# Kernel optimization log

Measured on AMD Instinct MI355X. Metric: run time of the kernel, lower is better.

The kernel has to match this reference:

```python
import jax, jax.numpy as jnp
import numpy as np

NEG_SLOPE = 0.2
RECON_W = 0.1
BN_EPS = 1e-5


def gat_conv(x, edge_index, W, a_src, a_dst, b):
    """PyG-style GATConv (eval mode, add_self_loops=True, concat heads).
    x: [N, F_in], W: [F_in, H*C], a_src/a_dst: [H, C], b: [H*C]."""
    N = x.shape[0]
    H, C = a_src.shape
    h = (x @ W).reshape(N, H, C)                      # [N,H,C]
    loop = jnp.arange(N, dtype=edge_index.dtype)
    src = jnp.concatenate([edge_index[0], loop])
    dst = jnp.concatenate([edge_index[1], loop])
    alpha_src = jnp.sum(h * a_src, axis=-1)           # [N,H]
    alpha_dst = jnp.sum(h * a_dst, axis=-1)           # [N,H]
    e = jax.nn.leaky_relu(alpha_src[src] + alpha_dst[dst], NEG_SLOPE)  # [E,H]
    # segment softmax over incoming edges of each destination node
    m = jax.ops.segment_max(e, dst, num_segments=N)
    e = jnp.exp(e - m[dst])
    s = jax.ops.segment_sum(e, dst, num_segments=N)
    p = e / s[dst]                                    # [E,H]
    out = jax.ops.segment_sum(p[:, :, None] * h[src], dst, num_segments=N)  # [N,H,C]
    return out.reshape(N, H * C) + b


def setup_inputs() -> dict:
    key = jax.random.key(0)
    ks = jax.random.split(key, 24)
    N, E = 100000, 800000
    F_in, hid, heads, n_cls, ctx_d, expl_d = 128, 32, 4, 10, 6, 32
    HC = hid * heads  # 128
    g = lambda k, shp, sc=0.1: jax.random.normal(k, shp, dtype=jnp.float32) * sc
    return {
        "x": jax.random.normal(ks[0], (N, F_in), dtype=jnp.float32),
        "edge_index": jax.random.randint(ks[1], (2, E), 0, N, dtype=jnp.int32),
        "context": jax.random.normal(ks[2], (N, ctx_d), dtype=jnp.float32),
        # GATConv 1: F_in -> hid, heads
        "W1": g(ks[3], (F_in, HC)), "a_src1": g(ks[4], (heads, hid)),
        "a_dst1": g(ks[5], (heads, hid)), "b1": g(ks[6], (HC,)),
        # BatchNorm1d(HC), eval mode
        "bn_gamma": jnp.ones((HC,), jnp.float32), "bn_beta": g(ks[7], (HC,)),
        "bn_mean": g(ks[8], (HC,)), "bn_var": jax.random.uniform(ks[9], (HC,), jnp.float32, 0.5, 1.5),
        # GATConv 2: HC -> hid, 1 head
        "W2": g(ks[10], (HC, hid)), "a_src2": g(ks[11], (1, hid)),
        "a_dst2": g(ks[12], (1, hid)), "b2": g(ks[13], (hid,)),
        # Reasoner MLP: ctx_d -> hid -> expl_d
        "rw1": g(ks[14], (ctx_d, hid)), "rb1": g(ks[15], (hid,)),
        "rw2": g(ks[16], (hid, expl_d)), "rb2": g(ks[17], (expl_d,)),
        # Decoder: expl_d -> hid
        "dw": g(ks[18], (expl_d, hid)), "db": g(ks[19], (hid,)),
        # Classifier: hid -> n_cls
        "cw": g(ks[20], (hid, n_cls)), "cb": g(ks[21], (n_cls,)),
    }


def reference(x, edge_index, context, W1, a_src1, a_dst1, b1,
              bn_gamma, bn_beta, bn_mean, bn_var,
              W2, a_src2, a_dst2, b2, rw1, rb1, rw2, rb2, dw, db, cw, cb):
    # layer 1: GAT -> BN(eval) -> ELU (dropout inactive in eval)
    h = gat_conv(x, edge_index, W1, a_src1, a_dst1, b1)
    h = (h - bn_mean) * jax.lax.rsqrt(bn_var + BN_EPS) * bn_gamma + bn_beta
    h = jax.nn.elu(h)
    # layer 2: GAT (1 head)
    h = gat_conv(h, edge_index, W2, a_src2, a_dst2, b2)  # [N, hid]
    # reasoner + decoder
    expl = jnp.maximum(context @ rw1 + rb1, 0.0) @ rw2 + rb2   # [N, expl_d]
    recon = expl @ dw + db                                     # [N, hid]
    combined = h + RECON_W * recon
    logits = combined @ cw + cb
    return jax.nn.log_softmax(logits, axis=1), expl
```

## Files before the change

### kernel.cpp

```cpp
#include <hip/hip_runtime.h>
#include <hip/hip_bf16.h>
#include <math.h>

#define NEG_SLOPE 0.2f
#define RECON_W 0.1f
#define BN_EPS 1e-5f
#define CAP 64

typedef __attribute__((ext_vector_type(8))) short short8;
typedef __attribute__((ext_vector_type(4))) float f32x4;

__device__ __forceinline__ float lrelu(float v) {
    return (v >= 0.f) ? v : NEG_SLOPE * v;
}
__device__ __forceinline__ unsigned short f2bf(float f) {
    unsigned int u = __float_as_uint(f);
    u = (u + 0x7fffu + ((u >> 16) & 1u)) >> 16;
    return (unsigned short)u;
}
__device__ __forceinline__ float bf2f(unsigned short u) {
    return __uint_as_float(((unsigned int)u) << 16);
}
__device__ __forceinline__ unsigned int pack2bf(float a, float b) {
    return (unsigned int)f2bf(a) | ((unsigned int)f2bf(b) << 16);
}
__device__ __forceinline__ void unpack2(unsigned int u, float& a, float& b) {
    a = bf2f((unsigned short)u);
    b = bf2f((unsigned short)(u >> 16));
}

__global__ __launch_bounds__(256) void prep_kernel(
    const float* __restrict__ W1, const float* __restrict__ W2,
    const float* __restrict__ b1, const float* __restrict__ g,
    const float* __restrict__ be, const float* __restrict__ m, const float* __restrict__ v,
    unsigned short* __restrict__ w1t, unsigned short* __restrict__ w2t,
    float* __restrict__ bnsc, float* __restrict__ bnsh) {
    int b = blockIdx.x, tid = threadIdx.x;
    if (b < 64) {
        int e = b * 256 + tid;
        w1t[e] = f2bf(W1[(e & 127) * 128 + (e >> 7)]);
    } else {
        #pragma unroll
        for (int it = 0; it < 16; it++) {
            int e = it * 256 + tid;
            w2t[e] = f2bf(W2[(e & 127) * 32 + (e >> 7)]);
        }
        if (tid < 128) {
            float s = rsqrtf(v[tid] + BN_EPS) * g[tid];
            bnsc[tid] = s;
            bnsh[tid] = (b1[tid] - m[tid]) * s + be[tid];
        }
    }
}

__global__ __launch_bounds__(256) void gemm1_mfma_kernel(
    const float* __restrict__ x, const unsigned short* __restrict__ w1t,
    const float* __restrict__ a_src, const float* __restrict__ a_dst,
    unsigned short* __restrict__ h1g, float* __restrict__ as1, float* __restrict__ ad1, int N,
    const int* __restrict__ esrc, const int* __restrict__ edst, int E,
    int* __restrict__ cnt, int* __restrict__ csrS) {
    __shared__ unsigned short sA[64 * 128];
    __shared__ unsigned short sBt[128 * 128];
    __shared__ float s_as[128], s_ad[128];
    int tid = threadIdx.x;
    int rowBase = blockIdx.x * 64;

    int bs0 = -1, bs1 = -1, bd0 = 0, bd1 = 0, bp0 = CAP, bp1 = CAP;
    int nb = gridDim.x;
    int epb = (E + nb - 1) / nb;
    int e0 = blockIdx.x * epb;
    int e1 = min(e0 + epb, E);
    {
        int e = e0 + tid;
        if (e < e1) { bs0 = esrc[e]; bd0 = edst[e]; }
        if (e + 256 < e1) { bs1 = esrc[e + 256]; bd1 = edst[e + 256]; }
        if (bs0 >= 0) bp0 = atomicAdd(&cnt[bd0], 1);
        if (bs1 >= 0) bp1 = atomicAdd(&cnt[bd1], 1);
    }

    if (tid < 128) { s_as[tid] = a_src[tid]; s_ad[tid] = a_dst[tid]; }
    #pragma unroll
    for (int u = 0; u < 8; u++) {
        int f = tid + u * 256;
        int r = f >> 5, cg = f & 31;
        int gr = rowBase + r;
        float4 vv = make_float4(0.f, 0.f, 0.f, 0.f);
        if (gr < N) vv = *(const float4*)(x + (size_t)gr * 128 + cg * 4);
        uint2 pk;
        pk.x = pack2bf(vv.x, vv.y);
        pk.y = pack2bf(vv.z, vv.w);
        ((uint2*)sA)[f] = pk;
    }
    #pragma unroll
    for (int u = 0; u < 8; u++) {
        int f = tid + u * 256;
        ((uint4*)sBt)[f] = ((const uint4*)w1t)[f];
    }
    __syncthreads();

    int lane = tid & 63;
    int w = tid >> 6;
    int quad = lane >> 4;
    int m16 = lane & 15;

    f32x4 acc[8];
    #pragma unroll
    for (int t = 0; t < 8; t++) acc[t] = (f32x4){0.f, 0.f, 0.f, 0.f};

    #pragma unroll
    for (int kc = 0; kc < 4; kc++) {
        int k0 = kc * 32 + quad * 8;
        short8 af = *(const short8*)(sA + ((w * 16 + m16) * 128 + k0));
        #pragma unroll
        for (int t = 0; t < 8; t++) {
            short8 bf = *(const short8*)(sBt + ((t * 16 + m16) * 128 + k0));
            acc[t] = __builtin_amdgcn_mfma_f32_16x16x32_bf16(af, bf, acc[t], 0, 0, 0);
        }
    }

    #pragma unroll
    for (int t = 0; t < 8; t++) {
        #pragma unroll
        for (int r = 0; r < 4; r++) {
            int row = w * 16 + quad * 4 + r;
            int col = t * 16 + m16;
            sA[row * 128 + col] = f2bf(acc[t][r]);
        }
    }
    __syncthreads();
    #pragma unroll
    for (int u = 0; u < 8; u++) {
        int f = tid + u * 256;
        int r = f >> 5, cg = f & 31;
        int gr = rowBase + r;
        if (gr < N) *(uint2*)(h1g + (size_t)gr * 128 + cg * 4) = ((const uint2*)sA)[f];
    }
    {
        int row = tid >> 2, head = tid & 3;
        int gr = rowBase + row;
        if (gr < N) {
            const unsigned int* rowp = (const unsigned int*)(sA + row * 128);
            float ps = 0.f, pd = 0.f;
            #pragma unroll
            for (int j = 0; j < 16; j++) {
                float f0, f1;
                unpack2(rowp[head * 16 + j], f0, f1);
                int c = head * 32 + j * 2;
                ps = fmaf(f0, s_as[c], fmaf(f1, s_as[c + 1], ps));
                pd = fmaf(f0, s_ad[c], fmaf(f1, s_ad[c + 1], pd));
            }
            as1[gr * 4 + head] = ps;
            ad1[gr * 4 + head] = pd;
        }
    }
    if (bs0 >= 0 && bp0 < CAP) csrS[(size_t)bd0 * CAP + bp0] = bs0;
    if (bs1 >= 0 && bp1 < CAP) csrS[(size_t)bd1 * CAP + bp1] = bs1;
    for (int e = e0 + tid + 512; e < e1; e += 256) {
        int s = esrc[e], d = edst[e];
        int pos = atomicAdd(&cnt[d], 1);
        if (pos < CAP) csrS[(size_t)d * CAP + pos] = s;
    }
}

__global__ __launch_bounds__(256) void agg1_kernel(
    const unsigned short* __restrict__ h1g,
    const float* __restrict__ as1, const float* __restrict__ ad1,
    const int* __restrict__ cnt, const int* __restrict__ csrS,
    const float* __restrict__ bnscale, const float* __restrict__ bnshift,
    unsigned short* __restrict__ h1p, int N) {
    __shared__ int   sSrc[16][CAP + 1];
    __shared__ float sW[16][CAP + 1][4];
    int tid = threadIdx.x;
    int nid = tid >> 4;
    int l   = tid & 15;
    int n = blockIdx.x * 16 + nid;
    bool alive = (n < N);
    int total = 0;

    if (alive) {
        int deg = min(cnt[n], CAP);
        total = deg + 1;
        float4 ad4 = *(const float4*)(ad1 + (size_t)n * 4);
        for (int slot = l; slot < total; slot += 16) {
            int s = (slot < deg) ? csrS[n * CAP + slot] : n;
            sSrc[nid][slot] = s;
            float4 a = *(const float4*)(as1 + (size_t)s * 4);
            float4 w4;
            w4.x = __expf(lrelu(a.x + ad4.x));
            w4.y = __expf(lrelu(a.y + ad4.y));
            w4.z = __expf(lrelu(a.z + ad4.z));
            w4.w = __expf(lrelu(a.w + ad4.w));
            *(float4*)(&sW[nid][slot][0]) = w4;
        }
    }
    __syncthreads();
    if (!alive) return;

    int hl = l >> 2;
    unsigned choff = (unsigned)(l << 3);
    const int* sS = sSrc[nid];
    const float* sWp = &sW[nid][0][0];

    float pa0 = 0.f, pa1 = 0.f, pa2 = 0.f, pa3 = 0.f;
    float pa4 = 0.f, pa5 = 0.f, pa6 = 0.f, pa7 = 0.f;
    float pb0 = 0.f, pb1 = 0.f, pb2 = 0.f, pb3 = 0.f;
    float pb4 = 0.f, pb5 = 0.f, pb6 = 0.f, pb7 = 0.f;
    float sa = 0.f, sb = 0.f;
    int j = 0;
    for (; j + 1 < total; j += 2) {
        int s0 = sS[j];
        int s1 = sS[j + 1];
        float w0 = sWp[(j << 2) + hl];
        float w1 = sWp[((j + 1) << 2) + hl];
        uint4 u0 = *(const uint4*)(h1g + (((unsigned)s0 << 7) + choff));
        uint4 u1 = *(const uint4*)(h1g + (((unsigned)s1 << 7) + choff));
        float f0, f1;
        unpack2(u0.x, f0, f1); pa0 = fmaf(w0, f0, pa0); pa1 = fmaf(w0, f1, pa1);
        unpack2(u0.y, f0, f1); pa2 = fmaf(w0, f0, pa2); pa3 = fmaf(w0, f1, pa3);
        unpack2(u0.z, f0, f1); pa4 = fmaf(w0, f0, pa4); pa5 = fmaf(w0, f1, pa5);
        unpack2(u0.w, f0, f1); pa6 = fmaf(w0, f0, pa6); pa7 = fmaf(w0, f1, pa7);
        sa += w0;
        unpack2(u1.x, f0, f1); pb0 = fmaf(w1, f0, pb0); pb1 = fmaf(w1, f1, pb1);
        unpack2(u1.y, f0, f1); pb2 = fmaf(w1, f0, pb2); pb3 = fmaf(w1, f1, pb3);
        unpack2(u1.z, f0, f1); pb4 = fmaf(w1, f0, pb4); pb5 = fmaf(w1, f1, pb5);
        unpack2(u1.w, f0, f1); pb6 = fmaf(w1, f0, pb6); pb7 = fmaf(w1, f1, pb7);
        sb += w1;
    }
    if (j < total) {
        int s0 = sS[j];
        float w0 = sWp[(j << 2) + hl];
        uint4 u0 = *(const uint4*)(h1g + (((unsigned)s0 << 7) + choff));
        float f0, f1;
        unpack2(u0.x, f0, f1); pa0 = fmaf(w0, f0, pa0); pa1 = fmaf(w0, f1, pa1);
        unpack2(u0.y, f0, f1); pa2 = fmaf(w0, f0, pa2); pa3 = fmaf(w0, f1, pa3);
        unpack2(u0.z, f0, f1); pa4 = fmaf(w0, f0, pa4); pa5 = fmaf(w0, f1, pa5);
        unpack2(u0.w, f0, f1); pa6 = fmaf(w0, f0, pa6); pa7 = fmaf(w0, f1, pa7);
        sa += w0;
    }
    float inv = 1.f / (sa + sb);
    float4 sc0 = *(const float4*)(bnscale + l * 8);
    float4 sc1 = *(const float4*)(bnscale + l * 8 + 4);
    float4 sh0 = *(const float4*)(bnshift + l * 8);
    float4 sh1 = *(const float4*)(bnshift + l * 8 + 4);
    float o0 = fmaf((pa0 + pb0) * inv, sc0.x, sh0.x);
    float o1 = fmaf((pa1 + pb1) * inv, sc0.y, sh0.y);
    float o2 = fmaf((pa2 + pb2) * inv, sc0.z, sh0.z);
    float o3 = fmaf((pa3 + pb3) * inv, sc0.w, sh0.w);
    float o4 = fmaf((pa4 + pb4) * inv, sc1.x, sh1.x);
    float o5 = fmaf((pa5 + pb5) * inv, sc1.y, sh1.y);
    float o6 = fmaf((pa6 + pb6) * inv, sc1.z, sh1.z);
    float o7 = fmaf((pa7 + pb7) * inv, sc1.w, sh1.w);
    o0 = (o0 > 0.f) ? o0 : expm1f(o0);
    o1 = (o1 > 0.f) ? o1 : expm1f(o1);
    o2 = (o2 > 0.f) ? o2 : expm1f(o2);
    o3 = (o3 > 0.f) ? o3 : expm1f(o3);
    o4 = (o4 > 0.f) ? o4 : expm1f(o4);
    o5 = (o5 > 0.f) ? o5 : expm1f(o5);
    o6 = (o6 > 0.f) ? o6 : expm1f(o6);
    o7 = (o7 > 0.f) ? o7 : expm1f(o7);
    uint4 pk;
    pk.x = pack2bf(o0, o1);
    pk.y = pack2bf(o2, o3);
    pk.z = pack2bf(o4, o5);
    pk.w = pack2bf(o6, o7);
    *(uint4*)(h1p + (size_t)n * 128 + l * 8) = pk;
}

__global__ __launch_bounds__(256) void gemm2_mfma_kernel(
    const unsigned short* __restrict__ A, const unsigned short* __restrict__ w2t,
    const float* __restrict__ a_src, const float* __restrict__ a_dst,
    unsigned short* __restrict__ h2g, float* __restrict__ as2, float* __restrict__ ad2, int N) {
    __shared__ unsigned short sA[64 * 128];
    __shared__ unsigned short sBt[32 * 128];
    __shared__ unsigned short sC[64 * 32];
    __shared__ float s_as[32], s_ad[32];
    int tid = threadIdx.x;
    int rowBase = blockIdx.x * 64;

    if (tid < 32) { s_as[tid] = a_src[tid]; s_ad[tid] = a_dst[tid]; }
    #pragma unroll
    for (int u = 0; u < 4; u++) {
        int f = tid + u * 256;
        int r = f >> 4, g = f & 15;
        int gr = rowBase + r;
        uint4 vv = make_uint4(0, 0, 0, 0);
        if (gr < N) vv = *(const uint4*)(A + (size_t)gr * 128 + g * 8);
        ((uint4*)sA)[f] = vv;
    }
    #pragma unroll
    for (int u = 0; u < 2; u++) {
        int f = tid + u * 256;
        ((uint4*)sBt)[f] = ((const uint4*)w2t)[f];
    }
    __syncthreads();

    int lane = tid & 63;
    int w = tid >> 6;
    int quad = lane >> 4;
    int m16 = lane & 15;

    f32x4 acc[2];
    acc[0] = (f32x4){0.f, 0.f, 0.f, 0.f};
    acc[1] = (f32x4){0.f, 0.f, 0.f, 0.f};
    #pragma unroll
    for (int kc = 0; kc < 4; kc++) {
        int k0 = kc * 32 + quad * 8;
        short8 af = *(const short8*)(sA + ((w * 16 + m16) * 128 + k0));
        #pragma unroll
        for (int t = 0; t < 2; t++) {
            short8 bf = *(const short8*)(sBt + ((t * 16 + m16) * 128 + k0));
            acc[t] = __builtin_amdgcn_mfma_f32_16x16x32_bf16(af, bf, acc[t], 0, 0, 0);
        }
    }
    #pragma unroll
    for (int t = 0; t < 2; t++) {
        #pragma unroll
        for (int r = 0; r < 4; r++) {
            int row = w * 16 + quad * 4 + r;
            sC[row * 32 + t * 16 + m16] = f2bf(acc[t][r]);
        }
    }
    __syncthreads();
    {
        int r = tid >> 2, g = tid & 3;
        int gr = rowBase + r;
        if (gr < N) *(uint4*)(h2g + (size_t)gr * 32 + g * 8) = ((const uint4*)sC)[tid];
    }
    if (tid < 64) {
        int gr = rowBase + tid;
        if (gr < N) {
            const unsigned int* rowp = (const unsigned int*)(sC + tid * 32);
            float ps = 0.f, pd = 0.f;
            #pragma unroll
            for (int j = 0; j < 16; j++) {
                float f0, f1;
                unpack2(rowp[j], f0, f1);
                ps = fmaf(f0, s_as[j * 2], fmaf(f1, s_as[j * 2 + 1], ps));
                pd = fmaf(f0, s_ad[j * 2], fmaf(f1, s_ad[j * 2 + 1], pd));
            }
            as2[gr] = ps;
            ad2[gr] = pd;
        }
    }
}

__global__ __launch_bounds__(256) void agg2_kernel(
    const unsigned short* __restrict__ h2g,
    const float* __restrict__ as2, const float* __restrict__ ad2,
    const int* __restrict__ cnt, const int* __restrict__ csrS,
    const float* __restrict__ b2, float* __restrict__ hl2, int N) {
    __shared__ int   sSrc[32][CAP + 1];
    __shared__ float sW[32][CAP + 1];
    int tid = threadIdx.x;
    int nid = tid >> 3;
    int l   = tid & 7;
    int n = blockIdx.x * 32 + nid;
    bool alive = (n < N);
    int total = 0;

    if (alive) {
        int deg = min(cnt[n], CAP);
        total = deg + 1;
        float ad = ad2[n];
        for (int slot = l; slot < total; slot += 8) {
            int s = (slot < deg) ? csrS[n * CAP + slot] : n;
            sSrc[nid][slot] = s;
            sW[nid][slot] = __expf(lrelu(as2[s] + ad));
        }
    }
    __syncthreads();
    if (!alive) return;

    unsigned choff = (unsigned)(l << 2);
    const int* sS = sSrc[nid];
    const float* sWp = sW[nid];

    float a0a = 0.f, a1a = 0.f, a2a = 0.f, a3a = 0.f, sa = 0.f;
    float a0b = 0.f, a1b = 0.f, a2b = 0.f, a3b = 0.f, sb = 0.f;
    int j = 0;
    for (; j + 1 < total; j += 2) {
        int s0 = sS[j];
        int s1 = sS[j + 1];
        float w0 = sWp[j];
        float w1 = sWp[j + 1];
        uint2 u0 = *(const uint2*)(h2g + (((unsigned)s0 << 5) + choff));
        uint2 u1 = *(const uint2*)(h2g + (((unsigned)s1 << 5) + choff));
        float f0, f1;
        unpack2(u0.x, f0, f1); a0a = fmaf(w0, f0, a0a); a1a = fmaf(w0, f1, a1a);
        unpack2(u0.y, f0, f1); a2a = fmaf(w0, f0, a2a); a3a = fmaf(w0, f1, a3a);
        sa += w0;
        unpack2(u1.x, f0, f1); a0b = fmaf(w1, f0, a0b); a1b = fmaf(w1, f1, a1b);
        unpack2(u1.y, f0, f1); a2b = fmaf(w1, f0, a2b); a3b = fmaf(w1, f1, a3b);
        sb += w1;
    }
    if (j < total) {
        int s0 = sS[j];
        float w0 = sWp[j];
        uint2 u0 = *(const uint2*)(h2g + (((unsigned)s0 << 5) + choff));
        float f0, f1;
        unpack2(u0.x, f0, f1); a0a = fmaf(w0, f0, a0a); a1a = fmaf(w0, f1, a1a);
        unpack2(u0.y, f0, f1); a2a = fmaf(w0, f0, a2a); a3a = fmaf(w0, f1, a3a);
        sa += w0;
    }
    float inv = 1.f / (sa + sb);
    float4 bb = *(const float4*)(b2 + l * 4);
    float4 o;
    o.x = (a0a + a0b) * inv + bb.x;
    o.y = (a1a + a1b) * inv + bb.y;
    o.z = (a2a + a2b) * inv + bb.z;
    o.w = (a3a + a3b) * inv + bb.w;
    *(float4*)(hl2 + (size_t)n * 32 + l * 4) = o;
}

__global__ __launch_bounds__(256) void head_kernel(
    const float* __restrict__ context, const float* __restrict__ hl2,
    const float* __restrict__ rw1, const float* __restrict__ rb1,
    const float* __restrict__ rw2, const float* __restrict__ rb2,
    const float* __restrict__ dw, const float* __restrict__ db,
    const float* __restrict__ cw, const float* __restrict__ cb,
    float* __restrict__ out_lsm, float* __restrict__ out_expl, int N) {
    __shared__ float s_rw1[192], s_rw2[1024], s_dw[1024], s_cw[320];
    __shared__ float s_rb1[32], s_rb2[32], s_db[32], s_cb[10];
    int tid = threadIdx.x;
    for (int i = tid; i < 192; i += 256) s_rw1[i] = rw1[i];
    for (int i = tid; i < 1024; i += 256) { s_rw2[i] = rw2[i]; s_dw[i] = dw[i]; }
    for (int i = tid; i < 320; i += 256) s_cw[i] = cw[i];
    if (tid < 32) { s_rb1[tid] = rb1[tid]; s_rb2[tid] = rb2[tid]; s_db[tid] = db[tid]; }
    if (tid < 10) s_cb[tid] = cb[tid];
    __syncthreads();
    int n = blockIdx.x * 256 + tid;
    if (n >= N) return;

    float ctx[6];
    #pragma unroll
    for (int i = 0; i < 6; i++) ctx[i] = context[(size_t)n * 6 + i];

    float t1[32];
    #pragma unroll
    for (int c = 0; c < 32; c++) t1[c] = s_rb1[c];
    #pragma unroll
    for (int i = 0; i < 6; i++) {
        float s = ctx[i];
        #pragma unroll
        for (int c = 0; c < 32; c++) t1[c] = fmaf(s, s_rw1[i * 32 + c], t1[c]);
    }
    #pragma unroll
    for (int c = 0; c < 32; c++) t1[c] = fmaxf(t1[c], 0.f);

    float ex[32];
    #pragma unroll
    for (int c = 0; c < 32; c++) ex[c] = s_rb2[c];
    #pragma unroll
    for (int c = 0; c < 32; c++) {
        float s = t1[c];
        #pragma unroll
        for (int c2 = 0; c2 < 32; c2++) ex[c2] = fmaf(s, s_rw2[c * 32 + c2], ex[c2]);
    }
    #pragma unroll
    for (int c = 0; c < 32; c += 4)
        *(float4*)(out_expl + (size_t)n * 32 + c) = make_float4(ex[c], ex[c + 1], ex[c + 2], ex[c + 3]);

    float rec[32];
    #pragma unroll
    for (int k = 0; k < 32; k++) rec[k] = s_db[k];
    #pragma unroll
    for (int c = 0; c < 32; c++) {
        float s = ex[c];
        #pragma unroll
        for (int k = 0; k < 32; k++) rec[k] = fmaf(s, s_dw[c * 32 + k], rec[k]);
    }
    float comb[32];
    #pragma unroll
    for (int k = 0; k < 32; k += 4) {
        float4 h = *(const float4*)(hl2 + (size_t)n * 32 + k);
        comb[k] = h.x + RECON_W * rec[k];
        comb[k + 1] = h.y + RECON_W * rec[k + 1];
        comb[k + 2] = h.z + RECON_W * rec[k + 2];
        comb[k + 3] = h.w + RECON_W * rec[k + 3];
    }
    float lg[10];
    #pragma unroll
    for (int j = 0; j < 10; j++) lg[j] = s_cb[j];
    #pragma unroll
    for (int k = 0; k < 32; k++) {
        float s = comb[k];
        #pragma unroll
        for (int j = 0; j < 10; j++) lg[j] = fmaf(s, s_cw[k * 10 + j], lg[j]);
    }
    float mx = lg[0];
    #pragma unroll
    for (int j = 1; j < 10; j++) mx = fmaxf(mx, lg[j]);
    float se = 0.f;
    #pragma unroll
    for (int j = 0; j < 10; j++) se += expf(lg[j] - mx);
    float lse = mx + logf(se);
    #pragma unroll
    for (int j = 0; j < 10; j++) out_lsm[(size_t)n * 10 + j] = lg[j] - lse;
}

extern "C" void kernel_launch(void* const* d_in, const int* in_sizes, int n_in,
                              void* d_out, int out_size, void* d_ws, size_t ws_size,
                              hipStream_t stream) {
    const float* x    = (const float*)d_in[0];
    const int* ei     = (const int*)d_in[1];
    const float* ctx  = (const float*)d_in[2];
    const float* W1   = (const float*)d_in[3];
    const float* a_s1 = (const float*)d_in[4];
    const float* a_d1 = (const float*)d_in[5];
    const float* b1   = (const float*)d_in[6];
    const float* bn_g = (const float*)d_in[7];
    const float* bn_b = (const float*)d_in[8];
    const float* bn_m = (const float*)d_in[9];
    const float* bn_v = (const float*)d_in[10];
    const float* W2   = (const float*)d_in[11];
    const float* a_s2 = (const float*)d_in[12];
    const float* a_d2 = (const float*)d_in[13];
    const float* b2   = (const float*)d_in[14];
    const float* rw1  = (const float*)d_in[15];
    const float* rb1  = (const float*)d_in[16];
    const float* rw2  = (const float*)d_in[17];
    const float* rb2  = (const float*)d_in[18];
    const float* dw   = (const float*)d_in[19];
    const float* db   = (const float*)d_in[20];
    const float* cw   = (const float*)d_in[21];
    const float* cb   = (const float*)d_in[22];

    int N = in_sizes[0] / 128;
    int E = in_sizes[1] / 2;
    const int* esrc = ei;
    const int* edst = ei + E;

    char* w = (char*)d_ws;
    auto alloc = [&](size_t bytes) {
        void* p = (void*)w;
        w += (bytes + 255) & ~(size_t)255;
        return p;
    };
    unsigned short* h1g = (unsigned short*)alloc((size_t)N * 128 * 2);
    unsigned short* h1p = (unsigned short*)alloc((size_t)N * 128 * 2);
    float* as1  = (float*)alloc((size_t)N * 4 * 4);
    float* ad1  = (float*)alloc((size_t)N * 4 * 4);
    float* as2  = (float*)alloc((size_t)N * 4);
    float* ad2  = (float*)alloc((size_t)N * 4);
    int* cnt    = (int*)alloc((size_t)N * 4);
    int* csrS   = (int*)alloc((size_t)N * CAP * 4);
    float* bnsc = (float*)alloc(128 * 4);
    float* bnsh = (float*)alloc(128 * 4);
    unsigned short* w1t = (unsigned short*)alloc(128 * 128 * 2);
    unsigned short* w2t = (unsigned short*)alloc(32 * 128 * 2);
    unsigned short* h2g = h1g;
    float* hl2 = (float*)(h1g + (size_t)N * 32);

    float* out0 = (float*)d_out;
    float* out1 = out0 + (size_t)N * 10;

    hipMemsetAsync(cnt, 0, (size_t)N * 4, stream);

    prep_kernel<<<65, 256, 0, stream>>>(W1, W2, b1, bn_g, bn_b, bn_m, bn_v,
                                        w1t, w2t, bnsc, bnsh);
    gemm1_mfma_kernel<<<(N + 63) / 64, 256, 0, stream>>>(x, w1t, a_s1, a_d1, h1g, as1, ad1, N,
                                                         esrc, edst, E, cnt, csrS);
    agg1_kernel<<<(N + 15) / 16, 256, 0, stream>>>(h1g, as1, ad1, cnt, csrS,
                                                   bnsc, bnsh, h1p, N);
    gemm2_mfma_kernel<<<(N + 63) / 64, 256, 0, stream>>>(h1p, w2t, a_s2, a_d2, h2g, as2, ad2, N);
    agg2_kernel<<<(N + 31) / 32, 256, 0, stream>>>(h2g, as2, ad2, cnt, csrS, b2, hl2, N);
    head_kernel<<<(N + 255) / 256, 256, 0, stream>>>(ctx, hl2, rw1, rb1, rw2, rb2,
                                                     dw, db, cw, cb, out0, out1, N);
}
```

Before: 297.7 us.

## Replace fixed-capacity padded adjacency with compact CSR built via count-scan-scatter

Switches the per-destination adjacency from a padded N*64 slot array to a compact CSR. A counting pass is folded into the prep kernel, followed by a two-kernel prefix scan that produces row pointers and write cursors. The gemm1 kernel then scatters edges into the compact array, and both aggregation kernels read contiguous neighbor ranges. This cuts the adjacency footprint and gives the aggregation reads better locality, at the cost of an extra atomic pass over all edges and two additional kernel launches.

```diff
diff --git a/kernel.cpp b/kernel.cpp
--- a/kernel.cpp
+++ b/kernel.cpp
@@ -34,12 +34,13 @@
     const float* __restrict__ b1, const float* __restrict__ g,
     const float* __restrict__ be, const float* __restrict__ m, const float* __restrict__ v,
     unsigned short* __restrict__ w1t, unsigned short* __restrict__ w2t,
-    float* __restrict__ bnsc, float* __restrict__ bnsh) {
+    float* __restrict__ bnsc, float* __restrict__ bnsh,
+    const int* __restrict__ edst, int E, int* __restrict__ cnt) {
     int b = blockIdx.x, tid = threadIdx.x;
     if (b < 64) {
         int e = b * 256 + tid;
         w1t[e] = f2bf(W1[(e & 127) * 128 + (e >> 7)]);
-    } else {
+    } else if (b == 64) {
         #pragma unroll
         for (int it = 0; it < 16; it++) {
             int e = it * 256 + tid;
@@ -50,6 +51,52 @@
             bnsc[tid] = s;
             bnsh[tid] = (b1[tid] - m[tid]) * s + be[tid];
         }
+    } else {
+        int cb = b - 65;
+        int stride = (gridDim.x - 65) * 256;
+        for (int e = cb * 256 + tid; e < E; e += stride) {
+            atomicAdd(&cnt[edst[e]], 1);
+        }
+    }
+}
+
+__global__ __launch_bounds__(256) void scanA_kernel(
+    const int* __restrict__ cnt, int* __restrict__ epre, int* __restrict__ bsum, int N) {
+    __shared__ int tmp[256];
+    int tid = threadIdx.x;
+    int i = blockIdx.x * 256 + tid;
+    int v = (i < N) ? cnt[i] : 0;
+    tmp[tid] = v;
+    __syncthreads();
+    #pragma unroll
+    for (int off = 1; off < 256; off <<= 1) {
+        int t = (tid >= off) ? tmp[tid - off] : 0;
+        __syncthreads();
+        tmp[tid] += t;
+        __syncthreads();
+    }
+    if (i < N) epre[i] = tmp[tid] - v;
+    if (tid == 255) bsum[blockIdx.x] = tmp[255];
+}
+
+__global__ __launch_bounds__(256) void scanBC_kernel(
+    const int* __restrict__ cnt, const int* __restrict__ epre, const int* __restrict__ bsum,
+    int* __restrict__ rowptr, int* __restrict__ wp, int N) {
+    __shared__ int ws[4];
+    int b = blockIdx.x, tid = threadIdx.x;
+    int acc = 0;
+    for (int j = tid; j < b; j += 256) acc += bsum[j];
+    #pragma unroll
+    for (int o = 1; o < 64; o <<= 1) acc += __shfl_xor(acc, o);
+    if ((tid & 63) == 0) ws[tid >> 6] = acc;
+    __syncthreads();
+    int off = ws[0] + ws[1] + ws[2] + ws[3];
+    int i = b * 256 + tid;
+    if (i < N) {
+        int r = off + epre[i];
+        rowptr[i] = r;
+        wp[i] = r;
+        if (i == N - 1) rowptr[N] = r + cnt[N - 1];
     }
 }
 
@@ -58,24 +105,25 @@
     const float* __restrict__ a_src, const float* __restrict__ a_dst,
     unsigned short* __restrict__ h1g, float* __restrict__ as1, float* __restrict__ ad1, int N,
     const int* __restrict__ esrc, const int* __restrict__ edst, int E,
-    int* __restrict__ cnt, int* __restrict__ csrS) {
+    int* __restrict__ wp, int* __restrict__ csrC) {
     __shared__ unsigned short sA[64 * 128];
     __shared__ unsigned short sBt[128 * 128];
     __shared__ float s_as[128], s_ad[128];
     int tid = threadIdx.x;
     int rowBase = blockIdx.x * 64;
 
-    int bs0 = -1, bs1 = -1, bd0 = 0, bd1 = 0, bp0 = CAP, bp1 = CAP;
+    int bs0 = -1, bs1 = -1, bp0 = 0, bp1 = 0;
     int nb = gridDim.x;
     int epb = (E + nb - 1) / nb;
     int e0 = blockIdx.x * epb;
     int e1 = min(e0 + epb, E);
     {
         int e = e0 + tid;
+        int bd0 = 0, bd1 = 0;
         if (e < e1) { bs0 = esrc[e]; bd0 = edst[e]; }
         if (e + 256 < e1) { bs1 = esrc[e + 256]; bd1 = edst[e + 256]; }
-        if (bs0 >= 0) bp0 = atomicAdd(&cnt[bd0], 1);
-        if (bs1 >= 0) bp1 = atomicAdd(&cnt[bd1], 1);
+        if (bs0 >= 0) bp0 = atomicAdd(&wp[bd0], 1);
+        if (bs1 >= 0) bp1 = atomicAdd(&wp[bd1], 1);
     }
 
     if (tid < 128) { s_as[tid] = a_src[tid]; s_ad[tid] = a_dst[tid]; }
@@ -153,19 +201,19 @@
             ad1[gr * 4 + head] = pd;
         }
     }
-    if (bs0 >= 0 && bp0 < CAP) csrS[(size_t)bd0 * CAP + bp0] = bs0;
-    if (bs1 >= 0 && bp1 < CAP) csrS[(size_t)bd1 * CAP + bp1] = bs1;
+    if (bs0 >= 0) csrC[bp0] = bs0;
+    if (bs1 >= 0) csrC[bp1] = bs1;
     for (int e = e0 + tid + 512; e < e1; e += 256) {
         int s = esrc[e], d = edst[e];
-        int pos = atomicAdd(&cnt[d], 1);
-        if (pos < CAP) csrS[(size_t)d * CAP + pos] = s;
+        int pos = atomicAdd(&wp[d], 1);
+        csrC[pos] = s;
     }
 }
 
 __global__ __launch_bounds__(256) void agg1_kernel(
     const unsigned short* __restrict__ h1g,
     const float* __restrict__ as1, const float* __restrict__ ad1,
-    const int* __restrict__ cnt, const int* __restrict__ csrS,
+    const int* __restrict__ rowptr, const int* __restrict__ csrC,
     const float* __restrict__ bnscale, const float* __restrict__ bnshift,
     unsigned short* __restrict__ h1p, int N) {
     __shared__ int   sSrc[16][CAP + 1];
@@ -178,11 +226,12 @@
     int total = 0;
 
     if (alive) {
-        int deg = min(cnt[n], CAP);
+        int beg = rowptr[n];
+        int deg = min(rowptr[n + 1] - beg, CAP);
         total = deg + 1;
         float4 ad4 = *(const float4*)(ad1 + (size_t)n * 4);
         for (int slot = l; slot < total; slot += 16) {
-            int s = (slot < deg) ? csrS[n * CAP + slot] : n;
+            int s = (slot < deg) ? csrC[beg + slot] : n;
             sSrc[nid][slot] = s;
             float4 a = *(const float4*)(as1 + (size_t)s * 4);
             float4 w4;
@@ -347,7 +396,7 @@
 __global__ __launch_bounds__(256) void agg2_kernel(
     const unsigned short* __restrict__ h2g,
     const float* __restrict__ as2, const float* __restrict__ ad2,
-    const int* __restrict__ cnt, const int* __restrict__ csrS,
+    const int* __restrict__ rowptr, const int* __restrict__ csrC,
     const float* __restrict__ b2, float* __restrict__ hl2, int N) {
     __shared__ int   sSrc[32][CAP + 1];
     __shared__ float sW[32][CAP + 1];
@@ -359,11 +408,12 @@
     int total = 0;
 
     if (alive) {
-        int deg = min(cnt[n], CAP);
+        int beg = rowptr[n];
+        int deg = min(rowptr[n + 1] - beg, CAP);
         total = deg + 1;
         float ad = ad2[n];
         for (int slot = l; slot < total; slot += 8) {
-            int s = (slot < deg) ? csrS[n * CAP + slot] : n;
+            int s = (slot < deg) ? csrC[beg + slot] : n;
             sSrc[nid][slot] = s;
             sW[nid][slot] = __expf(lrelu(as2[s] + ad));
         }
@@ -543,7 +593,12 @@
     float* as2  = (float*)alloc((size_t)N * 4);
     float* ad2  = (float*)alloc((size_t)N * 4);
     int* cnt    = (int*)alloc((size_t)N * 4);
-    int* csrS   = (int*)alloc((size_t)N * CAP * 4);
+    int* rowptr = (int*)alloc(((size_t)N + 1) * 4);
+    int* wp     = (int*)alloc((size_t)N * 4);
+    int* epre   = (int*)alloc((size_t)N * 4);
+    int SB = (N + 255) / 256;
+    int* bsum   = (int*)alloc((size_t)SB * 4);
+    int* csrC   = (int*)alloc((size_t)E * 4);
     float* bnsc = (float*)alloc(128 * 4);
     float* bnsh = (float*)alloc(128 * 4);
     unsigned short* w1t = (unsigned short*)alloc(128 * 128 * 2);
@@ -556,14 +611,17 @@
 
     hipMemsetAsync(cnt, 0, (size_t)N * 4, stream);
 
-    prep_kernel<<<65, 256, 0, stream>>>(W1, W2, b1, bn_g, bn_b, bn_m, bn_v,
-                                        w1t, w2t, bnsc, bnsh);
+    int countBlocks = (E + 255) / 256;
+    prep_kernel<<<65 + countBlocks, 256, 0, stream>>>(
+        W1, W2, b1, bn_g, bn_b, bn_m, bn_v, w1t, w2t, bnsc, bnsh, edst, E, cnt);
+    scanA_kernel<<<SB, 256, 0, stream>>>(cnt, epre, bsum, N);
+    scanBC_kernel<<<SB, 256, 0, stream>>>(cnt, epre, bsum, rowptr, wp, N);
     gemm1_mfma_kernel<<<(N + 63) / 64, 256, 0, stream>>>(x, w1t, a_s1, a_d1, h1g, as1, ad1, N,
-                                                         esrc, edst, E, cnt, csrS);
-    agg1_kernel<<<(N + 15) / 16, 256, 0, stream>>>(h1g, as1, ad1, cnt, csrS,
+                                                         esrc, edst, E, wp, csrC);
+    agg1_kernel<<<(N + 15) / 16, 256, 0, stream>>>(h1g, as1, ad1, rowptr, csrC,
                                                    bnsc, bnsh, h1p, N);
     gemm2_mfma_kernel<<<(N + 63) / 64, 256, 0, stream>>>(h1p, w2t, a_s2, a_d2, h2g, as2, ad2, N);
-    agg2_kernel<<<(N + 31) / 32, 256, 0, stream>>>(h2g, as2, ad2, cnt, csrS, b2, hl2, N);
+    agg2_kernel<<<(N + 31) / 32, 256, 0, stream>>>(h2g, as2, ad2, rowptr, csrC, b2, hl2, N);
     head_kernel<<<(N + 255) / 256, 256, 0, stream>>>(ctx, hl2, rw1, rb1, rw2, rb2,
                                                      dw, db, cw, cb, out0, out1, N);
 }
```

Result: slower. 333.3 us (+12.0%).
